# Optimization experiments

Hardware: AMD Instinct MI355X
Metric: run time of the kernel (lower is better)

## Reference

```python
import jax, jax.numpy as jnp
import numpy as np

THR = 0.2
TEMPERATURE = 0.1
BORDER = 2
C = 256


def _interior_mask(h, w, b):
    # flattened [h*w] bool mask, False within b of any border of the (h, w) grid
    vh = (jnp.arange(h) >= b) & (jnp.arange(h) < h - b)
    vw = (jnp.arange(w) >= b) & (jnp.arange(w) < w - b)
    return (vh[:, None] & vw[None, :]).reshape(-1)


def setup_inputs() -> dict:
    key = jax.random.key(0)
    k0, k1, kw, kb = jax.random.split(key, 4)
    B, L, S = 2, 4800, 4800
    feat_c0 = jax.random.normal(k0, (B, L, C), dtype=jnp.float32)
    feat_c1 = jax.random.normal(k1, (B, S, C), dtype=jnp.float32)
    # nn.Linear(256, 256) params
    W = jax.random.normal(kw, (C, C), dtype=jnp.float32) / np.sqrt(C)
    b = jax.random.normal(kb, (C,), dtype=jnp.float32) * 0.01
    return {"feat_c0": feat_c0, "feat_c1": feat_c1, "W": W, "b": b,
            "h0c": 60, "w0c": 80, "h1c": 60, "w1c": 80}


def reference(feat_c0, feat_c1, W, b, h0c, w0c, h1c, w1c):
    # final_proj: y = x @ W^T + b, then scale by sqrt(C)
    scale = feat_c0.shape[-1] ** 0.5
    f0 = (feat_c0 @ W.T + b) / scale          # [B, L, C]
    f1 = (feat_c1 @ W.T + b) / scale          # [B, S, C]
    sim = jnp.einsum('nlc,nsc->nls', f0, f1) / TEMPERATURE  # [B, L, S]

    conf_0to1 = jax.nn.softmax(sim, axis=2)   # row softmax
    conf_1to0 = jax.nn.softmax(sim, axis=1)   # column softmax

    # mutual-argmax + threshold mask
    mask = (conf_0to1 > THR) & (conf_0to1 == conf_0to1.max(axis=2, keepdims=True))
    mask = mask | ((conf_1to0 > THR) & (conf_1to0 == conf_1to0.max(axis=1, keepdims=True)))

    # border suppression (equivalent to mask_border on [B,h0,w0,h1,w1])
    mask = mask & _interior_mask(h0c, w0c, BORDER)[None, :, None]
    mask = mask & _interior_mask(h1c, w1c, BORDER)[None, None, :]

    # mconf at kept positions (training path: max of both confidences), dense masked form
    mconf = jnp.where(mask, jnp.maximum(conf_0to1, conf_1to0), 0.0)
    return jnp.stack([conf_0to1, conf_1to0, mconf])  # [3, B, L, S]
```

## Files before the change

kernel.cpp:

```cpp
#include <hip/hip_runtime.h>
#include <hip/hip_bf16.h>

#define B_ 2
#define L_ 4800
#define S_ 4800
#define C_ 256
#define NT_ 75
#define BL_ (B_ * L_)
#define BS_ (B_ * S_)
#define BLS ((size_t)B_ * L_ * S_)

constexpr float kLOG2E = 1.4426950408889634f;

typedef __bf16 bf16x8 __attribute__((ext_vector_type(8)));
typedef float f32x4 __attribute__((ext_vector_type(4)));

static __device__ __forceinline__ f32x4 mfma16(bf16x8 a, bf16x8 b, f32x4 c) {
    return __builtin_amdgcn_mfma_f32_16x16x32_bf16(a, b, c, 0, 0, 0);
}

static __device__ __forceinline__ bf16x8 load_cvt8(const float* __restrict__ p) {
    float4 a = *(const float4*)p;
    float4 b = *(const float4*)(p + 4);
    bf16x8 r;
    r[0] = (__bf16)a.x; r[1] = (__bf16)a.y; r[2] = (__bf16)a.z; r[3] = (__bf16)a.w;
    r[4] = (__bf16)b.x; r[5] = (__bf16)b.y; r[6] = (__bf16)b.z; r[7] = (__bf16)b.w;
    return r;
}

__global__ __launch_bounds__(256) void proj_kernel(
    const float* __restrict__ x0, const float* __restrict__ x1,
    const float* __restrict__ W, const float* __restrict__ bias,
    __hip_bfloat16* __restrict__ y0, __hip_bfloat16* __restrict__ y1) {
    const float* __restrict__ x = (blockIdx.z == 0) ? x0 : x1;
    __hip_bfloat16* __restrict__ y = (blockIdx.z == 0) ? y0 : y1;

    int lane = threadIdx.x & 63, wid = threadIdx.x >> 6;
    int m = lane & 15, q = lane >> 4;
    int r0 = blockIdx.x * 64 + wid * 16;
    int c0 = blockIdx.y * 16;

    f32x4 acc = {0.f, 0.f, 0.f, 0.f};
    for (int kk = 0; kk < 8; ++kk) {
        bf16x8 a = load_cvt8(x + (size_t)(r0 + m) * C_ + kk * 32 + q * 8);
        bf16x8 b = load_cvt8(W + (size_t)(c0 + m) * C_ + kk * 32 + q * 8);
        acc = mfma16(a, b, acc);
    }
    float bv = bias[c0 + m];
#pragma unroll
    for (int i = 0; i < 4; ++i) {
        int row = q * 4 + i;
        y[(size_t)(r0 + row) * C_ + c0 + m] = __float2bfloat16((acc[i] + bv) * 0.0625f);
    }
}

static __device__ __forceinline__ void sim_tile(
    const __hip_bfloat16* __restrict__ A, const __hip_bfloat16* __restrict__ Bp,
    int r0, int c0, int mi, int q, f32x4 acc[2][2]) {
#pragma unroll
    for (int kk = 0; kk < 8; ++kk) {
        int ko = kk * 32 + q * 8;
        bf16x8 a0 = *(const bf16x8*)(A + (size_t)(r0 + mi) * C_ + ko);
        bf16x8 a1 = *(const bf16x8*)(A + (size_t)(r0 + 16 + mi) * C_ + ko);
        bf16x8 b0 = *(const bf16x8*)(Bp + (size_t)(c0 + mi) * C_ + ko);
        bf16x8 b1 = *(const bf16x8*)(Bp + (size_t)(c0 + 16 + mi) * C_ + ko);
        acc[0][0] = mfma16(a0, b0, acc[0][0]);
        acc[0][1] = mfma16(a0, b1, acc[0][1]);
        acc[1][0] = mfma16(a1, b0, acc[1][0]);
        acc[1][1] = mfma16(a1, b1, acc[1][1]);
    }
}

__global__ __launch_bounds__(256) void simstat_kernel(
    const __hip_bfloat16* __restrict__ f0, const __hip_bfloat16* __restrict__ f1,
    float* __restrict__ rowPM, float* __restrict__ rowPZ,
    float* __restrict__ colPM, float* __restrict__ colPZ) {
    int b = blockIdx.z;
    int lane = threadIdx.x & 63, wid = threadIdx.x >> 6;
    int wm = wid & 1, wn = wid >> 1;
    int mi = lane & 15, q = lane >> 4;
    int r0 = blockIdx.x * 64 + wm * 32;
    int c0 = blockIdx.y * 64 + wn * 32;

    const __hip_bfloat16* __restrict__ A = f0 + (size_t)b * L_ * C_;
    const __hip_bfloat16* __restrict__ Bp = f1 + (size_t)b * S_ * C_;

    f32x4 acc[2][2] = {};
    sim_tile(A, Bp, r0, c0, mi, q, acc);

    float v[2][2][4], e[2][2][4];
#pragma unroll
    for (int tm = 0; tm < 2; ++tm)
#pragma unroll
        for (int tn = 0; tn < 2; ++tn)
#pragma unroll
            for (int i = 0; i < 4; ++i) {
                float x = acc[tm][tn][i] * 10.0f;
                v[tm][tn][i] = x;
                e[tm][tn][i] = exp2f(x * kLOG2E);
            }

    float rm8[2][4], rz8[2][4];
#pragma unroll
    for (int tm = 0; tm < 2; ++tm)
#pragma unroll
        for (int i = 0; i < 4; ++i) {
            float m = fmaxf(v[tm][0][i], v[tm][1][i]);
            float z = e[tm][0][i] + e[tm][1][i];
#pragma unroll
            for (int d = 1; d < 16; d <<= 1) {
                m = fmaxf(m, __shfl_xor(m, d));
                z += __shfl_xor(z, d);
            }
            rm8[tm][i] = m; rz8[tm][i] = z;
        }

    float cm2[2], cz2[2];
#pragma unroll
    for (int tn = 0; tn < 2; ++tn) {
        float m = -3.0e38f, z = 0.f;
#pragma unroll
        for (int tm = 0; tm < 2; ++tm)
#pragma unroll
            for (int i = 0; i < 4; ++i) {
                m = fmaxf(m, v[tm][tn][i]);
                z += e[tm][tn][i];
            }
#pragma unroll
        for (int d = 16; d < 64; d <<= 1) {
            m = fmaxf(m, __shfl_xor(m, d));
            z += __shfl_xor(z, d);
        }
        cm2[tn] = m; cz2[tn] = z;
    }

    __shared__ float lRM[2][64], lRZ[2][64], lCM[2][64], lCZ[2][64];
    if (mi == 0) {
#pragma unroll
        for (int tm = 0; tm < 2; ++tm)
#pragma unroll
            for (int i = 0; i < 4; ++i) {
                int rl = wm * 32 + tm * 16 + q * 4 + i;
                lRM[wn][rl] = rm8[tm][i];
                lRZ[wn][rl] = rz8[tm][i];
            }
    }
    if (q == 0) {
#pragma unroll
        for (int tn = 0; tn < 2; ++tn) {
            int cl = wn * 32 + tn * 16 + mi;
            lCM[wm][cl] = cm2[tn];
            lCZ[wm][cl] = cz2[tn];
        }
    }
    __syncthreads();

    int t = threadIdx.x;
    if (t < 64) {
        float m = fmaxf(lRM[0][t], lRM[1][t]);
        float z = lRZ[0][t] + lRZ[1][t];
        size_t o = (size_t)blockIdx.y * BL_ + (size_t)b * L_ + blockIdx.x * 64 + t;
        rowPM[o] = m; rowPZ[o] = z;
    } else if (t < 128) {
        int c = t - 64;
        float m = fmaxf(lCM[0][c], lCM[1][c]);
        float z = lCZ[0][c] + lCZ[1][c];
        size_t o = (size_t)blockIdx.x * BS_ + (size_t)b * S_ + blockIdx.y * 64 + c;
        colPM[o] = m; colPZ[o] = z;
    }
}

__global__ __launch_bounds__(256) void stats_reduce_kernel(
    const float* __restrict__ rowPM, const float* __restrict__ rowPZ,
    const float* __restrict__ colPM, const float* __restrict__ colPZ,
    const int* __restrict__ ph0, const int* __restrict__ pw0,
    const int* __restrict__ ph1, const int* __restrict__ pw1,
    float* __restrict__ rowM, float* __restrict__ rowRZ, float* __restrict__ oklA,
    float* __restrict__ colM, float* __restrict__ colRZ, float* __restrict__ oksA) {
    int idx = blockIdx.x * 256 + threadIdx.x;
    if (idx < BL_) {
        float m = -3.0e38f, z = 0.f;
        for (int j = 0; j < NT_; ++j) {
            m = fmaxf(m, rowPM[(size_t)j * BL_ + idx]);
            z += rowPZ[(size_t)j * BL_ + idx];
        }
        rowM[idx] = m;
        rowRZ[idx] = 1.0f / z;
        int l = idx % L_;
        int h0 = ph0[0], w0 = pw0[0];
        int i0 = l / w0, j0 = l - i0 * w0;
        oklA[idx] = ((i0 >= 2) & (i0 < h0 - 2) & (j0 >= 2) & (j0 < w0 - 2)) ? 1.f : 0.f;
    } else if (idx < BL_ + BS_) {
        int c = idx - BL_;
        float m = -3.0e38f, z = 0.f;
        for (int j = 0; j < NT_; ++j) {
            m = fmaxf(m, colPM[(size_t)j * BS_ + c]);
            z += colPZ[(size_t)j * BS_ + c];
        }
        colM[c] = m;
        colRZ[c] = 1.0f / z;
        int s = c % S_;
        int h1 = ph1[0], w1 = pw1[0];
        int i1 = s / w1, j1 = s - i1 * w1;
        oksA[c] = ((i1 >= 2) & (i1 < h1 - 2) & (j1 >= 2) & (j1 < w1 - 2)) ? 1.f : 0.f;
    }
}

__global__ __launch_bounds__(256) void final_kernel(
    const __hip_bfloat16* __restrict__ f0, const __hip_bfloat16* __restrict__ f1,
    const float* __restrict__ rowM, const float* __restrict__ rowRZ, const float* __restrict__ oklA,
    const float* __restrict__ colM, const float* __restrict__ colRZ, const float* __restrict__ oksA,
    float* __restrict__ out) {
    int b = blockIdx.z;
    int lane = threadIdx.x & 63, wid = threadIdx.x >> 6;
    int wm = wid & 1, wn = wid >> 1;
    int mi = lane & 15, q = lane >> 4;
    int r0 = blockIdx.x * 64 + wm * 32;
    int c0 = blockIdx.y * 64 + wn * 32;

    __shared__ float sRM[64], sRZ[64], sOkl[64], sCM[64], sCRZ[64], sOks[64];
    int t = threadIdx.x;
    if (t < 64) {
        int r = b * L_ + blockIdx.x * 64 + t;
        sRM[t] = rowM[r]; sRZ[t] = rowRZ[r]; sOkl[t] = oklA[r];
    } else if (t < 128) {
        int c = b * S_ + blockIdx.y * 64 + (t - 64);
        sCM[t - 64] = colM[c]; sCRZ[t - 64] = colRZ[c]; sOks[t - 64] = oksA[c];
    }

    const __hip_bfloat16* __restrict__ A = f0 + (size_t)b * L_ * C_;
    const __hip_bfloat16* __restrict__ Bp = f1 + (size_t)b * S_ * C_;
    f32x4 acc[2][2] = {};
    sim_tile(A, Bp, r0, c0, mi, q, acc);

    __syncthreads();

#pragma unroll
    for (int tm = 0; tm < 2; ++tm)
#pragma unroll
        for (int tn = 0; tn < 2; ++tn)
#pragma unroll
            for (int i = 0; i < 4; ++i) {
                int rl = wm * 32 + tm * 16 + q * 4 + i;
                int cl = wn * 32 + tn * 16 + mi;
                float v = acc[tm][tn][i] * 10.0f;
                float e = exp2f(v * kLOG2E);
                float c0v = e * sRZ[rl];
                float c1v = e * sCRZ[cl];
                bool mk = ((c0v > 0.2f) & (v == sRM[rl])) | ((c1v > 0.2f) & (v == sCM[cl]));
                float mc = mk ? fmaxf(c0v, c1v) * sOkl[rl] * sOks[cl] : 0.f;
                size_t o = ((size_t)(b * L_ + blockIdx.x * 64 + rl)) * S_ + blockIdx.y * 64 + cl;
                __builtin_nontemporal_store(c0v, &out[o]);
                __builtin_nontemporal_store(c1v, &out[o + BLS]);
                __builtin_nontemporal_store(mc, &out[o + 2 * BLS]);
            }
}

extern "C" void kernel_launch(void* const* d_in, const int* in_sizes, int n_in,
                              void* d_out, int out_size, void* d_ws, size_t ws_size,
                              hipStream_t stream) {
    const float* feat0 = (const float*)d_in[0];
    const float* feat1 = (const float*)d_in[1];
    const float* W = (const float*)d_in[2];
    const float* bias = (const float*)d_in[3];
    const int* ph0 = (const int*)d_in[4];
    const int* pw0 = (const int*)d_in[5];
    const int* ph1 = (const int*)d_in[6];
    const int* pw1 = (const int*)d_in[7];
    float* out = (float*)d_out;

    char* ws = (char*)d_ws;
    size_t off = 0;
    auto alloc = [&](size_t bytes) { char* p = ws + off; off = (off + bytes + 255) & ~(size_t)255; return p; };
    __hip_bfloat16* f0 = (__hip_bfloat16*)alloc((size_t)B_ * L_ * C_ * 2);
    __hip_bfloat16* f1 = (__hip_bfloat16*)alloc((size_t)B_ * S_ * C_ * 2);
    float* rowPM = (float*)alloc((size_t)NT_ * BL_ * 4);
    float* rowPZ = (float*)alloc((size_t)NT_ * BL_ * 4);
    float* colPM = (float*)alloc((size_t)NT_ * BS_ * 4);
    float* colPZ = (float*)alloc((size_t)NT_ * BS_ * 4);
    float* rowM = (float*)alloc((size_t)BL_ * 4);
    float* rowRZ = (float*)alloc((size_t)BL_ * 4);
    float* oklA = (float*)alloc((size_t)BL_ * 4);
    float* colM = (float*)alloc((size_t)BS_ * 4);
    float* colRZ = (float*)alloc((size_t)BS_ * 4);
    float* oksA = (float*)alloc((size_t)BS_ * 4);
    (void)ws_size; (void)in_sizes; (void)n_in; (void)out_size;

    proj_kernel<<<dim3(150, 16, 2), 256, 0, stream>>>(feat0, feat1, W, bias, f0, f1);
    simstat_kernel<<<dim3(NT_, NT_, B_), 256, 0, stream>>>(f0, f1, rowPM, rowPZ, colPM, colPZ);
    stats_reduce_kernel<<<dim3(75), 256, 0, stream>>>(rowPM, rowPZ, colPM, colPZ,
                                                      ph0, pw0, ph1, pw1,
                                                      rowM, rowRZ, oklA, colM, colRZ, oksA);
    final_kernel<<<dim3(NT_, NT_, B_), 256, 0, stream>>>(f0, f1, rowM, rowRZ, oklA,
                                                         colM, colRZ, oksA, out);
}
```

Measured before the change: 870.8 us.

## Store the similarity matrix once and stream the final outputs elementwise

The stats kernel now writes the scaled similarity matrix to a workspace buffer as fp32, using larger 96x96 tiles with a 3x3 MFMA fragment grid per wave. The final kernel no longer recomputes the bf16 GEMM. It becomes a vectorized elementwise pass that reads the stored sim values plus the row and column statistics and writes the three outputs. This removes the second GEMM, and the larger tiles improve operand reuse. The cost is an extra roughly 184 MB fp32 write and read through HBM, and some idle threads in the final kernel's grid.

```diff
diff --git a/kernel.cpp b/kernel.cpp
--- a/kernel.cpp
+++ b/kernel.cpp
@@ -5,7 +5,7 @@
 #define L_ 4800
 #define S_ 4800
 #define C_ 256
-#define NT_ 75
+#define NT2_ 50
 #define BL_ (B_ * L_)
 #define BS_ (B_ * S_)
 #define BLS ((size_t)B_ * L_ * S_)
@@ -54,118 +54,128 @@
     }
 }
 
-static __device__ __forceinline__ void sim_tile(
-    const __hip_bfloat16* __restrict__ A, const __hip_bfloat16* __restrict__ Bp,
-    int r0, int c0, int mi, int q, f32x4 acc[2][2]) {
-#pragma unroll
-    for (int kk = 0; kk < 8; ++kk) {
-        int ko = kk * 32 + q * 8;
-        bf16x8 a0 = *(const bf16x8*)(A + (size_t)(r0 + mi) * C_ + ko);
-        bf16x8 a1 = *(const bf16x8*)(A + (size_t)(r0 + 16 + mi) * C_ + ko);
-        bf16x8 b0 = *(const bf16x8*)(Bp + (size_t)(c0 + mi) * C_ + ko);
-        bf16x8 b1 = *(const bf16x8*)(Bp + (size_t)(c0 + 16 + mi) * C_ + ko);
-        acc[0][0] = mfma16(a0, b0, acc[0][0]);
-        acc[0][1] = mfma16(a0, b1, acc[0][1]);
-        acc[1][0] = mfma16(a1, b0, acc[1][0]);
-        acc[1][1] = mfma16(a1, b1, acc[1][1]);
-    }
-}
-
 __global__ __launch_bounds__(256) void simstat_kernel(
     const __hip_bfloat16* __restrict__ f0, const __hip_bfloat16* __restrict__ f1,
+    float* __restrict__ sim,
     float* __restrict__ rowPM, float* __restrict__ rowPZ,
     float* __restrict__ colPM, float* __restrict__ colPZ) {
     int b = blockIdx.z;
     int lane = threadIdx.x & 63, wid = threadIdx.x >> 6;
     int wm = wid & 1, wn = wid >> 1;
     int mi = lane & 15, q = lane >> 4;
-    int r0 = blockIdx.x * 64 + wm * 32;
-    int c0 = blockIdx.y * 64 + wn * 32;
+    int r0 = blockIdx.x * 96 + wm * 48;
+    int c0 = blockIdx.y * 96 + wn * 48;
 
     const __hip_bfloat16* __restrict__ A = f0 + (size_t)b * L_ * C_;
     const __hip_bfloat16* __restrict__ Bp = f1 + (size_t)b * S_ * C_;
 
-    f32x4 acc[2][2] = {};
-    sim_tile(A, Bp, r0, c0, mi, q, acc);
-
-    float v[2][2][4], e[2][2][4];
-#pragma unroll
-    for (int tm = 0; tm < 2; ++tm)
-#pragma unroll
-        for (int tn = 0; tn < 2; ++tn)
-#pragma unroll
-            for (int i = 0; i < 4; ++i) {
-                float x = acc[tm][tn][i] * 10.0f;
-                v[tm][tn][i] = x;
-                e[tm][tn][i] = exp2f(x * kLOG2E);
-            }
-
-    float rm8[2][4], rz8[2][4];
-#pragma unroll
-    for (int tm = 0; tm < 2; ++tm)
+    f32x4 acc[3][3] = {};
+#pragma unroll
+    for (int kk = 0; kk < 8; ++kk) {
+        int ko = kk * 32 + q * 8;
+        bf16x8 af[3], bf[3];
+#pragma unroll
+        for (int m = 0; m < 3; ++m)
+            af[m] = *(const bf16x8*)(A + (size_t)(r0 + m * 16 + mi) * C_ + ko);
+#pragma unroll
+        for (int n = 0; n < 3; ++n)
+            bf[n] = *(const bf16x8*)(Bp + (size_t)(c0 + n * 16 + mi) * C_ + ko);
+#pragma unroll
+        for (int m = 0; m < 3; ++m)
+#pragma unroll
+            for (int n = 0; n < 3; ++n)
+                acc[m][n] = mfma16(af[m], bf[n], acc[m][n]);
+    }
+
+    float v[3][3][4], e[3][3][4];
+#pragma unroll
+    for (int m = 0; m < 3; ++m)
+#pragma unroll
+        for (int n = 0; n < 3; ++n)
+#pragma unroll
+            for (int i = 0; i < 4; ++i) {
+                float x = acc[m][n][i] * 10.0f;
+                v[m][n][i] = x;
+                e[m][n][i] = exp2f(x * kLOG2E);
+            }
+
+    float* __restrict__ simb = sim + (size_t)b * L_ * S_;
+#pragma unroll
+    for (int m = 0; m < 3; ++m)
+#pragma unroll
+        for (int n = 0; n < 3; ++n)
+#pragma unroll
+            for (int i = 0; i < 4; ++i) {
+                size_t o = (size_t)(r0 + m * 16 + q * 4 + i) * S_ + c0 + n * 16 + mi;
+                __builtin_nontemporal_store(v[m][n][i], &simb[o]);
+            }
+
+    float rm[3][4], rz[3][4];
+#pragma unroll
+    for (int m = 0; m < 3; ++m)
 #pragma unroll
         for (int i = 0; i < 4; ++i) {
-            float m = fmaxf(v[tm][0][i], v[tm][1][i]);
-            float z = e[tm][0][i] + e[tm][1][i];
+            float mx = fmaxf(fmaxf(v[m][0][i], v[m][1][i]), v[m][2][i]);
+            float zz = e[m][0][i] + e[m][1][i] + e[m][2][i];
 #pragma unroll
             for (int d = 1; d < 16; d <<= 1) {
-                m = fmaxf(m, __shfl_xor(m, d));
-                z += __shfl_xor(z, d);
-            }
-            rm8[tm][i] = m; rz8[tm][i] = z;
-        }
-
-    float cm2[2], cz2[2];
-#pragma unroll
-    for (int tn = 0; tn < 2; ++tn) {
-        float m = -3.0e38f, z = 0.f;
-#pragma unroll
-        for (int tm = 0; tm < 2; ++tm)
-#pragma unroll
-            for (int i = 0; i < 4; ++i) {
-                m = fmaxf(m, v[tm][tn][i]);
-                z += e[tm][tn][i];
+                mx = fmaxf(mx, __shfl_xor(mx, d));
+                zz += __shfl_xor(zz, d);
+            }
+            rm[m][i] = mx; rz[m][i] = zz;
+        }
+
+    float cm[3], cz[3];
+#pragma unroll
+    for (int n = 0; n < 3; ++n) {
+        float mx = -3.0e38f, zz = 0.f;
+#pragma unroll
+        for (int m = 0; m < 3; ++m)
+#pragma unroll
+            for (int i = 0; i < 4; ++i) {
+                mx = fmaxf(mx, v[m][n][i]);
+                zz += e[m][n][i];
             }
 #pragma unroll
         for (int d = 16; d < 64; d <<= 1) {
-            m = fmaxf(m, __shfl_xor(m, d));
-            z += __shfl_xor(z, d);
-        }
-        cm2[tn] = m; cz2[tn] = z;
-    }
-
-    __shared__ float lRM[2][64], lRZ[2][64], lCM[2][64], lCZ[2][64];
+            mx = fmaxf(mx, __shfl_xor(mx, d));
+            zz += __shfl_xor(zz, d);
+        }
+        cm[n] = mx; cz[n] = zz;
+    }
+
+    __shared__ float lRM[2][96], lRZ[2][96], lCM[2][96], lCZ[2][96];
     if (mi == 0) {
 #pragma unroll
-        for (int tm = 0; tm < 2; ++tm)
-#pragma unroll
-            for (int i = 0; i < 4; ++i) {
-                int rl = wm * 32 + tm * 16 + q * 4 + i;
-                lRM[wn][rl] = rm8[tm][i];
-                lRZ[wn][rl] = rz8[tm][i];
+        for (int m = 0; m < 3; ++m)
+#pragma unroll
+            for (int i = 0; i < 4; ++i) {
+                int rl = wm * 48 + m * 16 + q * 4 + i;
+                lRM[wn][rl] = rm[m][i];
+                lRZ[wn][rl] = rz[m][i];
             }
     }
     if (q == 0) {
 #pragma unroll
-        for (int tn = 0; tn < 2; ++tn) {
-            int cl = wn * 32 + tn * 16 + mi;
-            lCM[wm][cl] = cm2[tn];
-            lCZ[wm][cl] = cz2[tn];
+        for (int n = 0; n < 3; ++n) {
+            int cl = wn * 48 + n * 16 + mi;
+            lCM[wm][cl] = cm[n];
+            lCZ[wm][cl] = cz[n];
         }
     }
     __syncthreads();
 
     int t = threadIdx.x;
-    if (t < 64) {
+    if (t < 96) {
         float m = fmaxf(lRM[0][t], lRM[1][t]);
         float z = lRZ[0][t] + lRZ[1][t];
-        size_t o = (size_t)blockIdx.y * BL_ + (size_t)b * L_ + blockIdx.x * 64 + t;
+        size_t o = (size_t)blockIdx.y * BL_ + (size_t)b * L_ + blockIdx.x * 96 + t;
         rowPM[o] = m; rowPZ[o] = z;
-    } else if (t < 128) {
-        int c = t - 64;
+    } else if (t < 192) {
+        int c = t - 96;
         float m = fmaxf(lCM[0][c], lCM[1][c]);
         float z = lCZ[0][c] + lCZ[1][c];
-        size_t o = (size_t)blockIdx.x * BS_ + (size_t)b * S_ + blockIdx.y * 64 + c;
+        size_t o = (size_t)blockIdx.x * BS_ + (size_t)b * S_ + blockIdx.y * 96 + c;
         colPM[o] = m; colPZ[o] = z;
     }
 }
@@ -180,7 +190,7 @@
     int idx = blockIdx.x * 256 + threadIdx.x;
     if (idx < BL_) {
         float m = -3.0e38f, z = 0.f;
-        for (int j = 0; j < NT_; ++j) {
+        for (int j = 0; j < NT2_; ++j) {
             m = fmaxf(m, rowPM[(size_t)j * BL_ + idx]);
             z += rowPZ[(size_t)j * BL_ + idx];
         }
@@ -193,7 +203,7 @@
     } else if (idx < BL_ + BS_) {
         int c = idx - BL_;
         float m = -3.0e38f, z = 0.f;
-        for (int j = 0; j < NT_; ++j) {
+        for (int j = 0; j < NT2_; ++j) {
             m = fmaxf(m, colPM[(size_t)j * BS_ + c]);
             z += colPZ[(size_t)j * BS_ + c];
         }
@@ -207,53 +217,41 @@
 }
 
 __global__ __launch_bounds__(256) void final_kernel(
-    const __hip_bfloat16* __restrict__ f0, const __hip_bfloat16* __restrict__ f1,
+    const float* __restrict__ sim,
     const float* __restrict__ rowM, const float* __restrict__ rowRZ, const float* __restrict__ oklA,
     const float* __restrict__ colM, const float* __restrict__ colRZ, const float* __restrict__ oksA,
     float* __restrict__ out) {
-    int b = blockIdx.z;
-    int lane = threadIdx.x & 63, wid = threadIdx.x >> 6;
-    int wm = wid & 1, wn = wid >> 1;
-    int mi = lane & 15, q = lane >> 4;
-    int r0 = blockIdx.x * 64 + wm * 32;
-    int c0 = blockIdx.y * 64 + wn * 32;
-
-    __shared__ float sRM[64], sRZ[64], sOkl[64], sCM[64], sCRZ[64], sOks[64];
-    int t = threadIdx.x;
-    if (t < 64) {
-        int r = b * L_ + blockIdx.x * 64 + t;
-        sRM[t] = rowM[r]; sRZ[t] = rowRZ[r]; sOkl[t] = oklA[r];
-    } else if (t < 128) {
-        int c = b * S_ + blockIdx.y * 64 + (t - 64);
-        sCM[t - 64] = colM[c]; sCRZ[t - 64] = colRZ[c]; sOks[t - 64] = oksA[c];
-    }
-
-    const __hip_bfloat16* __restrict__ A = f0 + (size_t)b * L_ * C_;
-    const __hip_bfloat16* __restrict__ Bp = f1 + (size_t)b * S_ * C_;
-    f32x4 acc[2][2] = {};
-    sim_tile(A, Bp, r0, c0, mi, q, acc);
-
-    __syncthreads();
-
-#pragma unroll
-    for (int tm = 0; tm < 2; ++tm)
-#pragma unroll
-        for (int tn = 0; tn < 2; ++tn)
-#pragma unroll
-            for (int i = 0; i < 4; ++i) {
-                int rl = wm * 32 + tm * 16 + q * 4 + i;
-                int cl = wn * 32 + tn * 16 + mi;
-                float v = acc[tm][tn][i] * 10.0f;
-                float e = exp2f(v * kLOG2E);
-                float c0v = e * sRZ[rl];
-                float c1v = e * sCRZ[cl];
-                bool mk = ((c0v > 0.2f) & (v == sRM[rl])) | ((c1v > 0.2f) & (v == sCM[cl]));
-                float mc = mk ? fmaxf(c0v, c1v) * sOkl[rl] * sOks[cl] : 0.f;
-                size_t o = ((size_t)(b * L_ + blockIdx.x * 64 + rl)) * S_ + blockIdx.y * 64 + cl;
-                __builtin_nontemporal_store(c0v, &out[o]);
-                __builtin_nontemporal_store(c1v, &out[o + BLS]);
-                __builtin_nontemporal_store(mc, &out[o + 2 * BLS]);
-            }
+    int s4 = blockIdx.x * 256 + threadIdx.x;
+    if (s4 >= S_ / 4) return;
+    int s = s4 * 4;
+    int rg = blockIdx.y;
+    int b = rg / L_;
+
+    float rm = rowM[rg], rrz = rowRZ[rg], okl = oklA[rg];
+
+    f32x4 vv = __builtin_nontemporal_load((const f32x4*)(sim + (size_t)rg * S_ + s));
+    int cb = b * S_ + s;
+    f32x4 cmv = *(const f32x4*)(colM + cb);
+    f32x4 crz = *(const f32x4*)(colRZ + cb);
+    f32x4 oks = *(const f32x4*)(oksA + cb);
+
+    f32x4 o0, o1, o2;
+#pragma unroll
+    for (int i = 0; i < 4; ++i) {
+        float v = vv[i];
+        float e = exp2f(v * kLOG2E);
+        float c0v = e * rrz;
+        float c1v = e * crz[i];
+        bool mk = ((c0v > 0.2f) & (v == rm)) | ((c1v > 0.2f) & (v == cmv[i]));
+        o0[i] = c0v;
+        o1[i] = c1v;
+        o2[i] = mk ? fmaxf(c0v, c1v) * okl * oks[i] : 0.f;
+    }
+
+    size_t o = (size_t)rg * S_ + s;
+    __builtin_nontemporal_store(o0, (f32x4*)(out + o));
+    __builtin_nontemporal_store(o1, (f32x4*)(out + o + BLS));
+    __builtin_nontemporal_store(o2, (f32x4*)(out + o + 2 * BLS));
 }
 
 extern "C" void kernel_launch(void* const* d_in, const int* in_sizes, int n_in,
@@ -274,10 +272,11 @@
     auto alloc = [&](size_t bytes) { char* p = ws + off; off = (off + bytes + 255) & ~(size_t)255; return p; };
     __hip_bfloat16* f0 = (__hip_bfloat16*)alloc((size_t)B_ * L_ * C_ * 2);
     __hip_bfloat16* f1 = (__hip_bfloat16*)alloc((size_t)B_ * S_ * C_ * 2);
-    float* rowPM = (float*)alloc((size_t)NT_ * BL_ * 4);
-    float* rowPZ = (float*)alloc((size_t)NT_ * BL_ * 4);
-    float* colPM = (float*)alloc((size_t)NT_ * BS_ * 4);
-    float* colPZ = (float*)alloc((size_t)NT_ * BS_ * 4);
+    float* sim = (float*)alloc(BLS * 4);
+    float* rowPM = (float*)alloc((size_t)NT2_ * BL_ * 4);
+    float* rowPZ = (float*)alloc((size_t)NT2_ * BL_ * 4);
+    float* colPM = (float*)alloc((size_t)NT2_ * BS_ * 4);
+    float* colPZ = (float*)alloc((size_t)NT2_ * BS_ * 4);
     float* rowM = (float*)alloc((size_t)BL_ * 4);
     float* rowRZ = (float*)alloc((size_t)BL_ * 4);
     float* oklA = (float*)alloc((size_t)BL_ * 4);
@@ -287,10 +286,10 @@
     (void)ws_size; (void)in_sizes; (void)n_in; (void)out_size;
 
     proj_kernel<<<dim3(150, 16, 2), 256, 0, stream>>>(feat0, feat1, W, bias, f0, f1);
-    simstat_kernel<<<dim3(NT_, NT_, B_), 256, 0, stream>>>(f0, f1, rowPM, rowPZ, colPM, colPZ);
+    simstat_kernel<<<dim3(NT2_, NT2_, B_), 256, 0, stream>>>(f0, f1, sim, rowPM, rowPZ, colPM, colPZ);
     stats_reduce_kernel<<<dim3(75), 256, 0, stream>>>(rowPM, rowPZ, colPM, colPZ,
                                                       ph0, pw0, ph1, pw1,
                                                       rowM, rowRZ, oklA, colM, colRZ, oksA);
-    final_kernel<<<dim3(NT_, NT_, B_), 256, 0, stream>>>(f0, f1, rowM, rowRZ, oklA,
-                                                         colM, colRZ, oksA, out);
-}
+    final_kernel<<<dim3(5, BL_), 256, 0, stream>>>(sim, rowM, rowRZ, oklA,
+                                                   colM, colRZ, oksA, out);
+}
```

New measurement: 786.0 us. -9.7%, faster.
